# Kernel tuning notes

Measured on AMD Instinct MI355X. Metric: run time of the kernel, lower is better.

Reference implementation:

```python
import jax, jax.numpy as jnp
import numpy as np

T, B, I, H, L = 1024, 64, 512, 512, 2


def _gru_layer(x_seq, h0, w_ih, w_hh, b_ih, b_hh):
    # x_seq: [T, B, in], h0: [B, H]
    # Precompute input-side gates for all timesteps in one big GEMM.
    gx = jnp.einsum('tbi,gi->tbg', x_seq, w_ih) + b_ih  # [T, B, 3H]

    def step(h, gx_t):
        gh = h @ w_hh.T + b_hh                 # [B, 3H]
        i_r, i_z, i_n = jnp.split(gx_t, 3, axis=-1)
        h_r, h_z, h_n = jnp.split(gh, 3, axis=-1)
        r = jax.nn.sigmoid(i_r + h_r)
        z = jax.nn.sigmoid(i_z + h_z)
        n = jnp.tanh(i_n + r * h_n)
        hy = n + z * (h - n)                   # newgate + inputgate*(hx - newgate)
        return hy, hy

    hT, out = jax.lax.scan(step, h0, gx)
    return out, hT  # out: [T, B, H]


def setup_inputs() -> dict:
    key = jax.random.key(0)
    ks = jax.random.split(key, 10)
    stdv = 1.0 / np.sqrt(H)
    u = lambda k, shp: jax.random.uniform(k, shp, jnp.float32, -stdv, stdv)
    return {
        'x': jax.random.normal(ks[0], (T, B, I), jnp.float32),
        'hx': jax.random.normal(ks[1], (L, B, H), jnp.float32),
        'w_ih_0': u(ks[2], (3 * H, I)),
        'w_hh_0': u(ks[3], (3 * H, H)),
        'b_ih_0': u(ks[4], (3 * H,)),
        'b_hh_0': u(ks[5], (3 * H,)),
        'w_ih_1': u(ks[6], (3 * H, H)),
        'w_hh_1': u(ks[7], (3 * H, H)),
        'b_ih_1': u(ks[8], (3 * H,)),
        'b_hh_1': u(ks[9], (3 * H,)),
    }


def reference(x, hx, w_ih_0, w_hh_0, b_ih_0, b_hh_0, w_ih_1, w_hh_1, b_ih_1, b_hh_1):
    out0, h0T = _gru_layer(x, hx[0], w_ih_0, w_hh_0, b_ih_0, b_hh_0)
    out1, h1T = _gru_layer(out0, hx[1], w_ih_1, w_hh_1, b_ih_1, b_hh_1)
    output = out1                         # [T, B, H] (batch_first=False)
    output_hs = jnp.stack([h0T, h1T], 0)  # [L, B, H]
    return output, output_hs
```

## Files before the change

kernel.cpp:

```cpp
#include <hip/hip_runtime.h>
#include <cstdint>
#include <cstddef>

#define T_N 1024
#define B_N 64
#define I_N 512
#define H_N 512
#define G3  (3*H_N)
#define NBLK 256

typedef _Float16 f16;
typedef _Float16 f16x2 __attribute__((ext_vector_type(2)));
typedef unsigned long long ull;

#define SLOT(d) (((d)+2)&1)
#define TAG1(d) ((((d)+2)>>1)&1)

__device__ __forceinline__ f16x2 mkh2(float a, float b) {
  f16x2 v; v.x = (_Float16)a; v.y = (_Float16)b; return v;
}
__device__ __forceinline__ f16x2 bch2(unsigned int u) {
  return __builtin_bit_cast(f16x2, u);
}
__device__ __forceinline__ float fdot2_(f16x2 a, f16x2 b, float c) {
#if __has_builtin(__builtin_amdgcn_fdot2)
  return __builtin_amdgcn_fdot2(a, b, c, false);
#else
  return fmaf((float)a.x, (float)b.x, fmaf((float)a.y, (float)b.y, c));
#endif
}
__device__ __forceinline__ float sigm_(float x) { return 1.f / (1.f + __expf(-x)); }
__device__ __forceinline__ float tanhf_(float x) {
  float xx = fminf(15.f, fmaxf(-15.f, x));
  float e = __expf(2.f * xx);
  return (e - 1.f) / (e + 1.f);
}

__global__ __launch_bounds__(256) void gemm_nt(
    const float* __restrict__ A,
    const float* __restrict__ W,
    const float* __restrict__ bias,
    float* __restrict__ C,
    int M, int N, int K)
{
  __shared__ float As[32][68];
  __shared__ float Ws[32][68];
  const int tid = threadIdx.x;
  const int n0 = blockIdx.x * 64;
  const int m0 = blockIdx.y * 64;
  const int ty = tid >> 4;
  const int tx = tid & 15;

  float acc[4][4];
#pragma unroll
  for (int i = 0; i < 4; ++i)
#pragma unroll
    for (int jj = 0; jj < 4; ++jj) acc[i][jj] = 0.f;

  for (int k0 = 0; k0 < K; k0 += 32) {
#pragma unroll
    for (int i = 0; i < 2; ++i) {
      int idx = tid + i * 256;
      int r   = idx >> 3;
      int c4  = idx & 7;
      float4 va = *(const float4*)(A + (size_t)(m0 + r) * K + k0 + c4 * 4);
      As[c4*4+0][r] = va.x; As[c4*4+1][r] = va.y;
      As[c4*4+2][r] = va.z; As[c4*4+3][r] = va.w;
      float4 vw = *(const float4*)(W + (size_t)(n0 + r) * K + k0 + c4 * 4);
      Ws[c4*4+0][r] = vw.x; Ws[c4*4+1][r] = vw.y;
      Ws[c4*4+2][r] = vw.z; Ws[c4*4+3][r] = vw.w;
    }
    __syncthreads();
#pragma unroll
    for (int k = 0; k < 32; ++k) {
      float4 a = *(const float4*)&As[k][ty * 4];
      float4 w = *(const float4*)&Ws[k][tx * 4];
      acc[0][0] += a.x*w.x; acc[0][1] += a.x*w.y; acc[0][2] += a.x*w.z; acc[0][3] += a.x*w.w;
      acc[1][0] += a.y*w.x; acc[1][1] += a.y*w.y; acc[1][2] += a.y*w.z; acc[1][3] += a.y*w.w;
      acc[2][0] += a.z*w.x; acc[2][1] += a.z*w.y; acc[2][2] += a.z*w.z; acc[2][3] += a.z*w.w;
      acc[3][0] += a.w*w.x; acc[3][1] += a.w*w.y; acc[3][2] += a.w*w.z; acc[3][3] += a.w*w.w;
    }
    __syncthreads();
  }

  float4 bv = *(const float4*)(bias + n0 + tx * 4);
#pragma unroll
  for (int i = 0; i < 4; ++i) {
    int row = m0 + ty * 4 + i;
    float4 o;
    o.x = acc[i][0] + bv.x; o.y = acc[i][1] + bv.y;
    o.z = acc[i][2] + bv.z; o.w = acc[i][3] + bv.w;
    *(float4*)(C + (size_t)row * N + n0 + tx * 4) = o;
  }
}

__global__ __launch_bounds__(256) void pack_h_init(
    const float* __restrict__ hx, f16* __restrict__ h0x, f16* __restrict__ h1x)
{
  int i = blockIdx.x * 256 + threadIdx.x;
  unsigned short a = __builtin_bit_cast(unsigned short, (f16)hx[i]) & 0xFFFEu;
  unsigned short b = __builtin_bit_cast(unsigned short, (f16)hx[B_N * H_N + i]) & 0xFFFEu;
  ((unsigned short*)h0x)[B_N * H_N + i] = a;
  ((unsigned short*)h1x)[B_N * H_N + i] = b;
}

__global__ __launch_bounds__(256) void conv_w(
    const float* __restrict__ whh0, const float* __restrict__ wih1,
    const float* __restrict__ whh1, uint4* __restrict__ wbuf)
{
  int gid = blockIdx.x * 256 + threadIdx.x;
  int idx = gid % 36, rem = gid / 36;
  int tid = rem % 256, j = rem / 256;
  int u = tid >> 4, s = tid & 15;
  int mat = idx / 12, q = (idx % 12) / 4, c = idx % 4;
  const float* src = mat == 0 ? whh0 : (mat == 1 ? wih1 : whh1);
  const float* p = src + (size_t)(q * H_N + 16 * j + u) * H_N + 8 * s + 128 * c;
  uint4 o;
  o.x = __builtin_bit_cast(unsigned int, mkh2(p[0], p[1]));
  o.y = __builtin_bit_cast(unsigned int, mkh2(p[2], p[3]));
  o.z = __builtin_bit_cast(unsigned int, mkh2(p[4], p[5]));
  o.w = __builtin_bit_cast(unsigned int, mkh2(p[6], p[7]));
  wbuf[gid] = o;
}

#define D4Q(acc, wv, vv)                               \
  acc = fdot2_(bch2((wv).x), bch2((vv).x), acc);       \
  acc = fdot2_(bch2((wv).y), bch2((vv).y), acc);       \
  acc = fdot2_(bch2((wv).z), bch2((vv).z), acc);       \
  acc = fdot2_(bch2((wv).w), bch2((vv).w), acc);

template <int NQ>
__device__ __forceinline__ void rscat8(float a[][8], float* r, int s) {
#pragma unroll
  for (int q = 0; q < NQ; ++q) {
    float k4[4];
#pragma unroll
    for (int i = 0; i < 4; ++i) {
      float snd = (s & 1) ? a[q][i] : a[q][4 + i];
      float kp  = (s & 1) ? a[q][4 + i] : a[q][i];
      k4[i] = kp + __shfl_xor(snd, 1);
    }
    float k2[2];
#pragma unroll
    for (int i = 0; i < 2; ++i) {
      float snd = (s & 2) ? k4[i] : k4[2 + i];
      float kp  = (s & 2) ? k4[2 + i] : k4[i];
      k2[i] = kp + __shfl_xor(snd, 2);
    }
    float snd = (s & 4) ? k2[0] : k2[1];
    float kp  = (s & 4) ? k2[1] : k2[0];
    float k1 = kp + __shfl_xor(snd, 4);
    r[q] = k1 + __shfl_xor(k1, 8);
  }
}

__global__ __launch_bounds__(256, 1) void gru_fused(
    const float* __restrict__ gx,
    const float* __restrict__ hx,
    const uint4* __restrict__ wbuf,
    const float* __restrict__ bih1, const float* __restrict__ bhh0,
    const float* __restrict__ bhh1,
    float* __restrict__ out,
    float* __restrict__ hT,
    f16* __restrict__ h0x, f16* __restrict__ h1x)
{
  __shared__ __align__(16) ull sh0q[2][1024];
  __shared__ __align__(16) ull sh1q[1024];
  __shared__ __align__(8) unsigned short pkA[128], pkB[128];

  const int tid = threadIdx.x;
  const int bid = blockIdx.x;
  const int g = bid & 7;
  const int j = bid >> 3;
  const int u = tid >> 4;
  const int s = tid & 15;
  const ull M = 0x0001000100010001ULL;

  uint4 wq[36];
  {
    const uint4* wp = wbuf + ((size_t)j * 256 + tid) * 36;
#pragma unroll
    for (int i = 0; i < 36; ++i) wq[i] = wp[i];
#pragma unroll
    for (int i = 0; i < 36; ++i)
      asm volatile("" : "+v"(wq[i].x), "+v"(wq[i].y), "+v"(wq[i].z), "+v"(wq[i].w));
  }

  const int bb   = 4 * (s & 1) + 2 * ((s >> 1) & 1) + ((s >> 2) & 1);
  const int unit = 16 * j + u;
  const int gbi  = 8 * g + bb;
  const float bR0 = bhh0[unit], bZ0 = bhh0[H_N + unit], bN0 = bhh0[2 * H_N + unit];
  const float bR1 = bih1[unit] + bhh1[unit];
  const float bZ1 = bih1[H_N + unit] + bhh1[H_N + unit];
  const float bN1x = bih1[2 * H_N + unit], bN1h = bhh1[2 * H_N + unit];
  float hv0 = hx[(size_t)gbi * H_N + unit];
  float hv1 = hx[(size_t)(B_N + gbi) * H_N + unit];

  for (int t = 0; t <= T_N + 1; ++t) {
    const bool runA = (t < T_N);
    const bool pollH0 = (t <= T_N);
    const bool runB = (t >= 2);
    const int cur = t & 1;

    const ull* s0 = (const ull*)h0x + (size_t)SLOT(t - 1) * 8192 + (size_t)(8 * g) * 128;
    const ull* s1 = (const ull*)h1x + (size_t)SLOT(t - 3) * 8192 + (size_t)(8 * g) * 128;
    const ull e0 = TAG1(t - 1) ? M : 0ULL;
    const ull e1 = TAG1(t - 3) ? M : 0ULL;
    ull v0[4], v1[4];
    bool k0[4] = {false, false, false, false};
    if (pollH0) {
#pragma unroll
      for (int e = 0; e < 4; ++e)
        v0[e] = __hip_atomic_load(s0 + e * 256 + tid, __ATOMIC_RELAXED, __HIP_MEMORY_SCOPE_AGENT);
    }
    if (runB) {
#pragma unroll
      for (int e = 0; e < 4; ++e)
        v1[e] = __hip_atomic_load(s1 + e * 256 + tid, __ATOMIC_RELAXED, __HIP_MEMORY_SCOPE_AGENT);
    }

    float ir0 = 0, iz0 = 0, in0 = 0;
    if (runA) {
      const float* p = gx + ((size_t)t * B_N + gbi) * G3 + unit;
      ir0 = p[0]; iz0 = p[H_N]; in0 = p[2 * H_N];
    }

    if (runB) {
      bool k1[4] = {false, false, false, false};
      for (;;) {
        bool all = true;
#pragma unroll
        for (int e = 0; e < 4; ++e) {
          if (!k1[e]) k1[e] = ((v1[e] & M) == e1);
          all = all && k1[e];
        }
        if (__all(all)) break;
        __builtin_amdgcn_s_sleep(1);
#pragma unroll
        for (int e = 0; e < 4; ++e)
          if (!k1[e]) v1[e] = __hip_atomic_load(s1 + e * 256 + tid, __ATOMIC_RELAXED, __HIP_MEMORY_SCOPE_AGENT);
      }
#pragma unroll
      for (int e = 0; e < 4; ++e) sh1q[e * 256 + tid] = v1[e];
    }
    __syncthreads();

    if (runB) {
      float aB[4][8];
#pragma unroll
      for (int q = 0; q < 4; ++q)
#pragma unroll
        for (int b8 = 0; b8 < 8; ++b8) aB[q][b8] = 0.f;
      const uint4* xp = (const uint4*)sh0q[cur ^ 1];
      const uint4* hp = (const uint4*)sh1q;
#pragma unroll
      for (int b8 = 0; b8 < 8; ++b8) {
        uint4 xc[4], hc[4];
#pragma unroll
        for (int c = 0; c < 4; ++c) { xc[c] = xp[b8 * 64 + s + 16 * c]; hc[c] = hp[b8 * 64 + s + 16 * c]; }
        float a0 = aB[0][b8], a1 = aB[1][b8], a2 = aB[2][b8], a3 = aB[3][b8];
#pragma unroll
        for (int c = 0; c < 4; ++c) {
          D4Q(a0, wq[12 + 0 * 4 + c], xc[c]); D4Q(a0, wq[24 + 0 * 4 + c], hc[c]);
          D4Q(a1, wq[12 + 1 * 4 + c], xc[c]); D4Q(a1, wq[24 + 1 * 4 + c], hc[c]);
          D4Q(a2, wq[12 + 2 * 4 + c], xc[c]);
          D4Q(a3, wq[24 + 2 * 4 + c], hc[c]);
        }
        aB[0][b8] = a0; aB[1][b8] = a1; aB[2][b8] = a2; aB[3][b8] = a3;
      }
      float rB[4];
      rscat8<4>(aB, rB, s);
      float r = sigm_(rB[0] + bR1);
      float z = sigm_(rB[1] + bZ1);
      float n = tanhf_(rB[2] + bN1x + r * (rB[3] + bN1h));
      float hy = n + z * (hv1 - n); hv1 = hy;
      if (s < 8) pkB[bb * 16 + u] = __builtin_bit_cast(unsigned short, (f16)hy);
    }

    if (pollH0) {
      for (;;) {
        bool all = true;
#pragma unroll
        for (int e = 0; e < 4; ++e) {
          if (!k0[e]) k0[e] = ((v0[e] & M) == e0);
          all = all && k0[e];
        }
        if (__all(all)) break;
        __builtin_amdgcn_s_sleep(1);
#pragma unroll
        for (int e = 0; e < 4; ++e)
          if (!k0[e]) v0[e] = __hip_atomic_load(s0 + e * 256 + tid, __ATOMIC_RELAXED, __HIP_MEMORY_SCOPE_AGENT);
      }
#pragma unroll
      for (int e = 0; e < 4; ++e) sh0q[cur][e * 256 + tid] = v0[e];
    }
    __syncthreads();

    if (runA) {
      float aA[3][8];
#pragma unroll
      for (int q = 0; q < 3; ++q)
#pragma unroll
        for (int b8 = 0; b8 < 8; ++b8) aA[q][b8] = 0.f;
      const uint4* xp = (const uint4*)sh0q[cur];
#pragma unroll
      for (int b8 = 0; b8 < 8; ++b8) {
        uint4 xc[4];
#pragma unroll
        for (int c = 0; c < 4; ++c) xc[c] = xp[b8 * 64 + s + 16 * c];
        float a0 = aA[0][b8], a1 = aA[1][b8], a2 = aA[2][b8];
#pragma unroll
        for (int c = 0; c < 4; ++c) {
          D4Q(a0, wq[0 * 4 + c], xc[c]);
          D4Q(a1, wq[1 * 4 + c], xc[c]);
          D4Q(a2, wq[2 * 4 + c], xc[c]);
        }
        aA[0][b8] = a0; aA[1][b8] = a1; aA[2][b8] = a2;
      }
      float rA[3];
      rscat8<3>(aA, rA, s);
      float r = sigm_(ir0 + rA[0] + bR0);
      float z = sigm_(iz0 + rA[1] + bZ0);
      float n = tanhf_(in0 + r * (rA[2] + bN0));
      float hy = n + z * (hv0 - n); hv0 = hy;
      if (s < 8) {
        pkA[bb * 16 + u] = __builtin_bit_cast(unsigned short, (f16)hy);
        if (t == T_N - 1) hT[(size_t)gbi * H_N + unit] = hy;
      }
    }
    __syncthreads();

    if (tid < 32) {
      if (runA) {
        ull v = ((const ull*)pkA)[tid];
        v = (v & ~M) | (TAG1(t) ? M : 0ULL);
        ull* dp = (ull*)h0x + (size_t)SLOT(t) * 8192
                + (size_t)(8 * g + (tid >> 2)) * 128 + 4 * j + (tid & 3);
        __hip_atomic_store(dp, v, __ATOMIC_RELAXED, __HIP_MEMORY_SCOPE_AGENT);
      }
    } else if (tid < 64) {
      if (runB) {
        const int l = tid - 32;
        ull v = ((const ull*)pkB)[l];
        f16x2 p0 = bch2((unsigned int)v), p1 = bch2((unsigned int)(v >> 32));
        float4 o = {(float)p0.x, (float)p0.y, (float)p1.x, (float)p1.y};
        float* op = out + ((size_t)(t - 2) * B_N + 8 * g + (l >> 2)) * H_N + 16 * j + 4 * (l & 3);
        *(float4*)op = o;
        if (t == T_N + 1)
          *(float4*)(hT + (size_t)(B_N + 8 * g + (l >> 2)) * H_N + 16 * j + 4 * (l & 3)) = o;
        if (t <= T_N) {
          v = (v & ~M) | (TAG1(t - 2) ? M : 0ULL);
          ull* dp = (ull*)h1x + (size_t)SLOT(t - 2) * 8192
                  + (size_t)(8 * g + (l >> 2)) * 128 + 4 * j + (l & 3);
          __hip_atomic_store(dp, v, __ATOMIC_RELAXED, __HIP_MEMORY_SCOPE_AGENT);
        }
      }
    }
  }
}

extern "C" void kernel_launch(void* const* d_in, const int* in_sizes, int n_in,
                              void* d_out, int out_size, void* d_ws, size_t ws_size,
                              hipStream_t stream)
{
  const float* x    = (const float*)d_in[0];
  const float* hx   = (const float*)d_in[1];
  const float* wih0 = (const float*)d_in[2];
  const float* whh0 = (const float*)d_in[3];
  const float* bih0 = (const float*)d_in[4];
  const float* bhh0 = (const float*)d_in[5];
  const float* wih1 = (const float*)d_in[6];
  const float* whh1 = (const float*)d_in[7];
  const float* bih1 = (const float*)d_in[8];
  const float* bhh1 = (const float*)d_in[9];
  float* out = (float*)d_out;

  float* gxb = (float*)d_ws;
  f16*   h0x = (f16*)(gxb + (size_t)T_N * B_N * G3);
  f16*   h1x = h0x + 2 * B_N * H_N;
  uint4* wbuf = (uint4*)(h1x + 2 * B_N * H_N);

  pack_h_init<<<128, 256, 0, stream>>>(hx, h0x, h1x);
  conv_w<<<(32 * 256 * 36) / 256, 256, 0, stream>>>(whh0, wih1, whh1, wbuf);

  dim3 gg(G3 / 64, (T_N * B_N) / 64);
  gemm_nt<<<gg, 256, 0, stream>>>(x, wih0, bih0, gxb, T_N * B_N, G3, I_N);

  gru_fused<<<NBLK, 256, 0, stream>>>(gxb, hx, wbuf,
                                      bih1, bhh0, bhh1,
                                      out, out + (size_t)T_N * B_N * H_N,
                                      h0x, h1x);
}
```

Before: 8.917 ms.

## Split GRU recurrence reduction across 512 threads with half the weights per thread

Each block of the persistent fused GRU kernel now runs 512 threads instead of 256. The per-thread register-resident weight slice shrinks from 36 to 18 uint4, and each hidden unit's dot product is split across 32 lanes instead of 16. The weight-packing kernel, the shared-memory access pattern and the shuffle reduction change to match, and the reduction gains one more xor-16 stage. The aim is to shorten the serial per-timestep dot-product chain and free registers for more latency hiding, at the cost of an extra shuffle level, more threads synchronising at each barrier, and more lanes sitting idle during the activation step.

```diff
diff --git a/kernel.cpp b/kernel.cpp
--- a/kernel.cpp
+++ b/kernel.cpp
@@ -109,12 +109,12 @@
     const float* __restrict__ whh1, uint4* __restrict__ wbuf)
 {
   int gid = blockIdx.x * 256 + threadIdx.x;
-  int idx = gid % 36, rem = gid / 36;
-  int tid = rem % 256, j = rem / 256;
-  int u = tid >> 4, s = tid & 15;
-  int mat = idx / 12, q = (idx % 12) / 4, c = idx % 4;
+  int idx = gid % 18, rem = gid / 18;
+  int tid = rem % 512, j = rem / 512;
+  int u = tid >> 5, s = tid & 31;
+  int mat = idx / 6, q = (idx % 6) / 2, c = idx % 2;
   const float* src = mat == 0 ? whh0 : (mat == 1 ? wih1 : whh1);
-  const float* p = src + (size_t)(q * H_N + 16 * j + u) * H_N + 8 * s + 128 * c;
+  const float* p = src + (size_t)(q * H_N + 16 * j + u) * H_N + 16 * s + 8 * c;
   uint4 o;
   o.x = __builtin_bit_cast(unsigned int, mkh2(p[0], p[1]));
   o.y = __builtin_bit_cast(unsigned int, mkh2(p[2], p[3]));
@@ -130,7 +130,7 @@
   acc = fdot2_(bch2((wv).w), bch2((vv).w), acc);
 
 template <int NQ>
-__device__ __forceinline__ void rscat8(float a[][8], float* r, int s) {
+__device__ __forceinline__ void rscat8w(float a[][8], float* r, int s) {
 #pragma unroll
   for (int q = 0; q < NQ; ++q) {
     float k4[4];
@@ -150,11 +150,12 @@
     float snd = (s & 4) ? k2[0] : k2[1];
     float kp  = (s & 4) ? k2[1] : k2[0];
     float k1 = kp + __shfl_xor(snd, 4);
-    r[q] = k1 + __shfl_xor(k1, 8);
-  }
-}
-
-__global__ __launch_bounds__(256, 1) void gru_fused(
+    k1 = k1 + __shfl_xor(k1, 8);
+    r[q] = k1 + __shfl_xor(k1, 16);
+  }
+}
+
+__global__ __launch_bounds__(512, 2) void gru_fused(
     const float* __restrict__ gx,
     const float* __restrict__ hx,
     const uint4* __restrict__ wbuf,
@@ -172,29 +173,34 @@
   const int bid = blockIdx.x;
   const int g = bid & 7;
   const int j = bid >> 3;
-  const int u = tid >> 4;
-  const int s = tid & 15;
+  const int u = tid >> 5;
+  const int s = tid & 31;
   const ull M = 0x0001000100010001ULL;
 
-  uint4 wq[36];
+  uint4 wq[18];
   {
-    const uint4* wp = wbuf + ((size_t)j * 256 + tid) * 36;
-#pragma unroll
-    for (int i = 0; i < 36; ++i) wq[i] = wp[i];
-#pragma unroll
-    for (int i = 0; i < 36; ++i)
+    const uint4* wp = wbuf + ((size_t)j * 512 + tid) * 18;
+#pragma unroll
+    for (int i = 0; i < 18; ++i) wq[i] = wp[i];
+#pragma unroll
+    for (int i = 0; i < 18; ++i)
       asm volatile("" : "+v"(wq[i].x), "+v"(wq[i].y), "+v"(wq[i].z), "+v"(wq[i].w));
   }
 
   const int bb   = 4 * (s & 1) + 2 * ((s >> 1) & 1) + ((s >> 2) & 1);
   const int unit = 16 * j + u;
   const int gbi  = 8 * g + bb;
-  const float bR0 = bhh0[unit], bZ0 = bhh0[H_N + unit], bN0 = bhh0[2 * H_N + unit];
-  const float bR1 = bih1[unit] + bhh1[unit];
-  const float bZ1 = bih1[H_N + unit] + bhh1[H_N + unit];
-  const float bN1x = bih1[2 * H_N + unit], bN1h = bhh1[2 * H_N + unit];
-  float hv0 = hx[(size_t)gbi * H_N + unit];
-  float hv1 = hx[(size_t)(B_N + gbi) * H_N + unit];
+  const bool wr  = (s < 8);
+  float bR0 = 0, bZ0 = 0, bN0 = 0, bR1 = 0, bZ1 = 0, bN1x = 0, bN1h = 0;
+  float hv0 = 0, hv1 = 0;
+  if (wr) {
+    bR0 = bhh0[unit]; bZ0 = bhh0[H_N + unit]; bN0 = bhh0[2 * H_N + unit];
+    bR1 = bih1[unit] + bhh1[unit];
+    bZ1 = bih1[H_N + unit] + bhh1[H_N + unit];
+    bN1x = bih1[2 * H_N + unit]; bN1h = bhh1[2 * H_N + unit];
+    hv0 = hx[(size_t)gbi * H_N + unit];
+    hv1 = hx[(size_t)(B_N + gbi) * H_N + unit];
+  }
 
   for (int t = 0; t <= T_N + 1; ++t) {
     const bool runA = (t < T_N);
@@ -206,42 +212,42 @@
     const ull* s1 = (const ull*)h1x + (size_t)SLOT(t - 3) * 8192 + (size_t)(8 * g) * 128;
     const ull e0 = TAG1(t - 1) ? M : 0ULL;
     const ull e1 = TAG1(t - 3) ? M : 0ULL;
-    ull v0[4], v1[4];
-    bool k0[4] = {false, false, false, false};
+    ull v0[2], v1[2];
+    bool k0[2] = {false, false};
     if (pollH0) {
 #pragma unroll
-      for (int e = 0; e < 4; ++e)
-        v0[e] = __hip_atomic_load(s0 + e * 256 + tid, __ATOMIC_RELAXED, __HIP_MEMORY_SCOPE_AGENT);
+      for (int e = 0; e < 2; ++e)
+        v0[e] = __hip_atomic_load(s0 + e * 512 + tid, __ATOMIC_RELAXED, __HIP_MEMORY_SCOPE_AGENT);
     }
     if (runB) {
 #pragma unroll
-      for (int e = 0; e < 4; ++e)
-        v1[e] = __hip_atomic_load(s1 + e * 256 + tid, __ATOMIC_RELAXED, __HIP_MEMORY_SCOPE_AGENT);
+      for (int e = 0; e < 2; ++e)
+        v1[e] = __hip_atomic_load(s1 + e * 512 + tid, __ATOMIC_RELAXED, __HIP_MEMORY_SCOPE_AGENT);
     }
 
     float ir0 = 0, iz0 = 0, in0 = 0;
-    if (runA) {
+    if (runA && wr) {
       const float* p = gx + ((size_t)t * B_N + gbi) * G3 + unit;
       ir0 = p[0]; iz0 = p[H_N]; in0 = p[2 * H_N];
     }
 
     if (runB) {
-      bool k1[4] = {false, false, false, false};
+      bool k1[2] = {false, false};
       for (;;) {
         bool all = true;
 #pragma unroll
-        for (int e = 0; e < 4; ++e) {
+        for (int e = 0; e < 2; ++e) {
           if (!k1[e]) k1[e] = ((v1[e] & M) == e1);
           all = all && k1[e];
         }
         if (__all(all)) break;
         __builtin_amdgcn_s_sleep(1);
 #pragma unroll
-        for (int e = 0; e < 4; ++e)
-          if (!k1[e]) v1[e] = __hip_atomic_load(s1 + e * 256 + tid, __ATOMIC_RELAXED, __HIP_MEMORY_SCOPE_AGENT);
-      }
-#pragma unroll
-      for (int e = 0; e < 4; ++e) sh1q[e * 256 + tid] = v1[e];
+        for (int e = 0; e < 2; ++e)
+          if (!k1[e]) v1[e] = __hip_atomic_load(s1 + e * 512 + tid, __ATOMIC_RELAXED, __HIP_MEMORY_SCOPE_AGENT);
+      }
+#pragma unroll
+      for (int e = 0; e < 2; ++e) sh1q[e * 512 + tid] = v1[e];
     }
     __syncthreads();
 
@@ -255,44 +261,49 @@
       const uint4* hp = (const uint4*)sh1q;
 #pragma unroll
       for (int b8 = 0; b8 < 8; ++b8) {
-        uint4 xc[4], hc[4];
-#pragma unroll
-        for (int c = 0; c < 4; ++c) { xc[c] = xp[b8 * 64 + s + 16 * c]; hc[c] = hp[b8 * 64 + s + 16 * c]; }
+        uint4 xc[2], hc[2];
+#pragma unroll
+        for (int c = 0; c < 2; ++c) {
+          xc[c] = xp[b8 * 64 + 2 * s + c];
+          hc[c] = hp[b8 * 64 + 2 * s + c];
+        }
         float a0 = aB[0][b8], a1 = aB[1][b8], a2 = aB[2][b8], a3 = aB[3][b8];
 #pragma unroll
-        for (int c = 0; c < 4; ++c) {
-          D4Q(a0, wq[12 + 0 * 4 + c], xc[c]); D4Q(a0, wq[24 + 0 * 4 + c], hc[c]);
-          D4Q(a1, wq[12 + 1 * 4 + c], xc[c]); D4Q(a1, wq[24 + 1 * 4 + c], hc[c]);
-          D4Q(a2, wq[12 + 2 * 4 + c], xc[c]);
-          D4Q(a3, wq[24 + 2 * 4 + c], hc[c]);
+        for (int c = 0; c < 2; ++c) {
+          D4Q(a0, wq[6 + c],  xc[c]); D4Q(a0, wq[12 + c], hc[c]);
+          D4Q(a1, wq[8 + c],  xc[c]); D4Q(a1, wq[14 + c], hc[c]);
+          D4Q(a2, wq[10 + c], xc[c]);
+          D4Q(a3, wq[16 + c], hc[c]);
         }
         aB[0][b8] = a0; aB[1][b8] = a1; aB[2][b8] = a2; aB[3][b8] = a3;
       }
       float rB[4];
-      rscat8<4>(aB, rB, s);
-      float r = sigm_(rB[0] + bR1);
-      float z = sigm_(rB[1] + bZ1);
-      float n = tanhf_(rB[2] + bN1x + r * (rB[3] + bN1h));
-      float hy = n + z * (hv1 - n); hv1 = hy;
-      if (s < 8) pkB[bb * 16 + u] = __builtin_bit_cast(unsigned short, (f16)hy);
+      rscat8w<4>(aB, rB, s);
+      if (wr) {
+        float r = sigm_(rB[0] + bR1);
+        float z = sigm_(rB[1] + bZ1);
+        float n = tanhf_(rB[2] + bN1x + r * (rB[3] + bN1h));
+        float hy = n + z * (hv1 - n); hv1 = hy;
+        pkB[bb * 16 + u] = __builtin_bit_cast(unsigned short, (f16)hy);
+      }
     }
 
     if (pollH0) {
       for (;;) {
         bool all = true;
 #pragma unroll
-        for (int e = 0; e < 4; ++e) {
+        for (int e = 0; e < 2; ++e) {
           if (!k0[e]) k0[e] = ((v0[e] & M) == e0);
           all = all && k0[e];
         }
         if (__all(all)) break;
         __builtin_amdgcn_s_sleep(1);
 #pragma unroll
-        for (int e = 0; e < 4; ++e)
-          if (!k0[e]) v0[e] = __hip_atomic_load(s0 + e * 256 + tid, __ATOMIC_RELAXED, __HIP_MEMORY_SCOPE_AGENT);
-      }
-#pragma unroll
-      for (int e = 0; e < 4; ++e) sh0q[cur][e * 256 + tid] = v0[e];
+        for (int e = 0; e < 2; ++e)
+          if (!k0[e]) v0[e] = __hip_atomic_load(s0 + e * 512 + tid, __ATOMIC_RELAXED, __HIP_MEMORY_SCOPE_AGENT);
+      }
+#pragma unroll
+      for (int e = 0; e < 2; ++e) sh0q[cur][e * 512 + tid] = v0[e];
     }
     __syncthreads();
 
@@ -305,25 +316,25 @@
       const uint4* xp = (const uint4*)sh0q[cur];
 #pragma unroll
       for (int b8 = 0; b8 < 8; ++b8) {
-        uint4 xc[4];
-#pragma unroll
-        for (int c = 0; c < 4; ++c) xc[c] = xp[b8 * 64 + s + 16 * c];
+        uint4 xc[2];
+        xc[0] = xp[b8 * 64 + 2 * s];
+        xc[1] = xp[b8 * 64 + 2 * s + 1];
         float a0 = aA[0][b8], a1 = aA[1][b8], a2 = aA[2][b8];
 #pragma unroll
-        for (int c = 0; c < 4; ++c) {
-          D4Q(a0, wq[0 * 4 + c], xc[c]);
-          D4Q(a1, wq[1 * 4 + c], xc[c]);
-          D4Q(a2, wq[2 * 4 + c], xc[c]);
+        for (int c = 0; c < 2; ++c) {
+          D4Q(a0, wq[0 + c], xc[c]);
+          D4Q(a1, wq[2 + c], xc[c]);
+          D4Q(a2, wq[4 + c], xc[c]);
         }
         aA[0][b8] = a0; aA[1][b8] = a1; aA[2][b8] = a2;
       }
       float rA[3];
-      rscat8<3>(aA, rA, s);
-      float r = sigm_(ir0 + rA[0] + bR0);
-      float z = sigm_(iz0 + rA[1] + bZ0);
-      float n = tanhf_(in0 + r * (rA[2] + bN0));
-      float hy = n + z * (hv0 - n); hv0 = hy;
-      if (s < 8) {
+      rscat8w<3>(aA, rA, s);
+      if (wr) {
+        float r = sigm_(ir0 + rA[0] + bR0);
+        float z = sigm_(iz0 + rA[1] + bZ0);
+        float n = tanhf_(in0 + r * (rA[2] + bN0));
+        float hy = n + z * (hv0 - n); hv0 = hy;
         pkA[bb * 16 + u] = __builtin_bit_cast(unsigned short, (f16)hy);
         if (t == T_N - 1) hT[(size_t)gbi * H_N + unit] = hy;
       }
@@ -381,12 +392,12 @@
   uint4* wbuf = (uint4*)(h1x + 2 * B_N * H_N);
 
   pack_h_init<<<128, 256, 0, stream>>>(hx, h0x, h1x);
-  conv_w<<<(32 * 256 * 36) / 256, 256, 0, stream>>>(whh0, wih1, whh1, wbuf);
+  conv_w<<<(32 * 512 * 18) / 256, 256, 0, stream>>>(whh0, wih1, whh1, wbuf);
 
   dim3 gg(G3 / 64, (T_N * B_N) / 64);
   gemm_nt<<<gg, 256, 0, stream>>>(x, wih0, bih0, gxb, T_N * B_N, G3, I_N);
 
-  gru_fused<<<NBLK, 256, 0, stream>>>(gxb, hx, wbuf,
+  gru_fused<<<NBLK, 512, 0, stream>>>(gxb, hx, wbuf,
                                       bih1, bhh0, bhh1,
                                       out, out + (size_t)T_N * B_N * H_N,
                                       h0x, h1x);
```

After: 10.01 ms. 12.2% more time.

## Split fused two-layer GRU into separate layer-0 and layer-1 block groups

Applied to the files above, without the earlier changes.

The persistent kernel now launches 512 blocks: half run layer 0 and half run layer 1, each holding only its own weights in registers, instead of every block interleaving both layers per step. The hidden-state exchange buffers grow from 2 to 8 slots, so layer 0 can run up to several steps ahead of layer 1, with a throttle poll on layer-1 progress to stop slot reuse. This aims to shorten each block's per-step critical path and lower register pressure, which allows more occupancy. The cost is twice as many resident blocks spinning on global flags, and the design relies on all 512 blocks being co-resident to avoid deadlock.

```diff
diff --git a/kernel.cpp b/kernel.cpp
--- a/kernel.cpp
+++ b/kernel.cpp
@@ -7,14 +7,13 @@
 #define I_N 512
 #define H_N 512
 #define G3  (3*H_N)
-#define NBLK 256
 
 typedef _Float16 f16;
 typedef _Float16 f16x2 __attribute__((ext_vector_type(2)));
 typedef unsigned long long ull;
 
-#define SLOT(d) (((d)+2)&1)
-#define TAG1(d) ((((d)+2)>>1)&1)
+#define S8(d) (((d)+8)&7)
+#define T8(d) ((((d)+8)>>3)&1)
 
 __device__ __forceinline__ f16x2 mkh2(float a, float b) {
   f16x2 v; v.x = (_Float16)a; v.y = (_Float16)b; return v;
@@ -100,8 +99,8 @@
   int i = blockIdx.x * 256 + threadIdx.x;
   unsigned short a = __builtin_bit_cast(unsigned short, (f16)hx[i]) & 0xFFFEu;
   unsigned short b = __builtin_bit_cast(unsigned short, (f16)hx[B_N * H_N + i]) & 0xFFFEu;
-  ((unsigned short*)h0x)[B_N * H_N + i] = a;
-  ((unsigned short*)h1x)[B_N * H_N + i] = b;
+  ((unsigned short*)h0x)[7 * B_N * H_N + i] = a;
+  ((unsigned short*)h1x)[7 * B_N * H_N + i] = b;
 }
 
 __global__ __launch_bounds__(256) void conv_w(
@@ -154,7 +153,23 @@
   }
 }
 
-__global__ __launch_bounds__(256, 1) void gru_fused(
+#define POLL4(vv, kk, sp, ee)                                                  \
+  for (;;) {                                                                   \
+    bool all_ = true;                                                          \
+    _Pragma("unroll")                                                          \
+    for (int e_ = 0; e_ < 4; ++e_) {                                           \
+      if (!kk[e_]) kk[e_] = ((vv[e_] & M) == ee);                              \
+      all_ = all_ && kk[e_];                                                   \
+    }                                                                          \
+    if (__all(all_)) break;                                                    \
+    __builtin_amdgcn_s_sleep(1);                                               \
+    _Pragma("unroll")                                                          \
+    for (int e_ = 0; e_ < 4; ++e_)                                             \
+      if (!kk[e_]) vv[e_] = __hip_atomic_load(sp + e_ * 256 + tid,             \
+                     __ATOMIC_RELAXED, __HIP_MEMORY_SCOPE_AGENT);              \
+  }
+
+__global__ __launch_bounds__(256) void gru_split(
     const float* __restrict__ gx,
     const float* __restrict__ hx,
     const uint4* __restrict__ wbuf,
@@ -164,196 +179,200 @@
     float* __restrict__ hT,
     f16* __restrict__ h0x, f16* __restrict__ h1x)
 {
-  __shared__ __align__(16) ull sh0q[2][1024];
+  __shared__ __align__(16) ull shq[1024];
   __shared__ __align__(16) ull sh1q[1024];
-  __shared__ __align__(8) unsigned short pkA[128], pkB[128];
+  __shared__ __align__(8) unsigned short pk[128];
 
   const int tid = threadIdx.x;
-  const int bid = blockIdx.x;
-  const int g = bid & 7;
-  const int j = bid >> 3;
+  const bool L0 = (blockIdx.x < 256);
+  const int lb = L0 ? blockIdx.x : blockIdx.x - 256;
+  const int g = lb & 7;
+  const int j = lb >> 3;
   const int u = tid >> 4;
   const int s = tid & 15;
   const ull M = 0x0001000100010001ULL;
 
-  uint4 wq[36];
-  {
-    const uint4* wp = wbuf + ((size_t)j * 256 + tid) * 36;
-#pragma unroll
-    for (int i = 0; i < 36; ++i) wq[i] = wp[i];
-#pragma unroll
-    for (int i = 0; i < 36; ++i)
-      asm volatile("" : "+v"(wq[i].x), "+v"(wq[i].y), "+v"(wq[i].z), "+v"(wq[i].w));
-  }
-
   const int bb   = 4 * (s & 1) + 2 * ((s >> 1) & 1) + ((s >> 2) & 1);
   const int unit = 16 * j + u;
   const int gbi  = 8 * g + bb;
-  const float bR0 = bhh0[unit], bZ0 = bhh0[H_N + unit], bN0 = bhh0[2 * H_N + unit];
-  const float bR1 = bih1[unit] + bhh1[unit];
-  const float bZ1 = bih1[H_N + unit] + bhh1[H_N + unit];
-  const float bN1x = bih1[2 * H_N + unit], bN1h = bhh1[2 * H_N + unit];
-  float hv0 = hx[(size_t)gbi * H_N + unit];
-  float hv1 = hx[(size_t)(B_N + gbi) * H_N + unit];
-
-  for (int t = 0; t <= T_N + 1; ++t) {
-    const bool runA = (t < T_N);
-    const bool pollH0 = (t <= T_N);
-    const bool runB = (t >= 2);
-    const int cur = t & 1;
-
-    const ull* s0 = (const ull*)h0x + (size_t)SLOT(t - 1) * 8192 + (size_t)(8 * g) * 128;
-    const ull* s1 = (const ull*)h1x + (size_t)SLOT(t - 3) * 8192 + (size_t)(8 * g) * 128;
-    const ull e0 = TAG1(t - 1) ? M : 0ULL;
-    const ull e1 = TAG1(t - 3) ? M : 0ULL;
-    ull v0[4], v1[4];
-    bool k0[4] = {false, false, false, false};
-    if (pollH0) {
+  const bool wr  = (s < 8);
+  const ull* h0u = (const ull*)h0x;
+  const ull* h1u = (const ull*)h1x;
+
+  if (L0) {
+    uint4 wq[12];
+    {
+      const uint4* wp = wbuf + ((size_t)j * 256 + tid) * 36;
+#pragma unroll
+      for (int i = 0; i < 12; ++i) wq[i] = wp[i];
+#pragma unroll
+      for (int i = 0; i < 12; ++i)
+        asm volatile("" : "+v"(wq[i].x), "+v"(wq[i].y), "+v"(wq[i].z), "+v"(wq[i].w));
+    }
+    float bR0 = 0, bZ0 = 0, bN0 = 0, hv0 = 0;
+    if (wr) {
+      bR0 = bhh0[unit]; bZ0 = bhh0[H_N + unit]; bN0 = bhh0[2 * H_N + unit];
+      hv0 = hx[(size_t)gbi * H_N + unit];
+    }
+
+    for (int t = 0; t < T_N; ++t) {
+      const ull* s0 = h0u + (size_t)S8(t - 1) * 8192 + (size_t)(8 * g) * 128;
+      const ull e0 = T8(t - 1) ? M : 0ULL;
+      ull v0[4]; bool k0[4] = {false, false, false, false};
 #pragma unroll
       for (int e = 0; e < 4; ++e)
         v0[e] = __hip_atomic_load(s0 + e * 256 + tid, __ATOMIC_RELAXED, __HIP_MEMORY_SCOPE_AGENT);
-    }
-    if (runB) {
-#pragma unroll
-      for (int e = 0; e < 4; ++e)
+      const bool thr = (t >= 7);
+      const ull* sT = h1u + (size_t)S8(t - 7) * 8192 + (size_t)(8 * g) * 128;
+      const ull eT = T8(t - 7) ? M : 0ULL;
+      ull vT[4]; bool kT[4] = {!thr, !thr, !thr, !thr};
+      if (thr) {
+#pragma unroll
+        for (int e = 0; e < 4; ++e)
+          vT[e] = __hip_atomic_load(sT + e * 256 + tid, __ATOMIC_RELAXED, __HIP_MEMORY_SCOPE_AGENT);
+      }
+      float ir0 = 0, iz0 = 0, in0 = 0;
+      if (wr) {
+        const float* p = gx + ((size_t)t * B_N + gbi) * G3 + unit;
+        ir0 = p[0]; iz0 = p[H_N]; in0 = p[2 * H_N];
+      }
+
+      POLL4(v0, k0, s0, e0)
+#pragma unroll
+      for (int e = 0; e < 4; ++e) shq[e * 256 + tid] = v0[e];
+      __syncthreads();
+
+      float aA[3][8];
+#pragma unroll
+      for (int q = 0; q < 3; ++q)
+#pragma unroll
+        for (int b8 = 0; b8 < 8; ++b8) aA[q][b8] = 0.f;
+      const uint4* xp = (const uint4*)shq;
+#pragma unroll
+      for (int b8 = 0; b8 < 8; ++b8) {
+        uint4 xc[4];
+#pragma unroll
+        for (int c = 0; c < 4; ++c) xc[c] = xp[b8 * 64 + s + 16 * c];
+        float a0 = aA[0][b8], a1 = aA[1][b8], a2 = aA[2][b8];
+#pragma unroll
+        for (int c = 0; c < 4; ++c) {
+          D4Q(a0, wq[0 + c], xc[c]);
+          D4Q(a1, wq[4 + c], xc[c]);
+          D4Q(a2, wq[8 + c], xc[c]);
+        }
+        aA[0][b8] = a0; aA[1][b8] = a1; aA[2][b8] = a2;
+      }
+      float rA[3];
+      rscat8<3>(aA, rA, s);
+      if (wr) {
+        float r = sigm_(ir0 + rA[0] + bR0);
+        float z = sigm_(iz0 + rA[1] + bZ0);
+        float n = tanhf_(in0 + r * (rA[2] + bN0));
+        float hy = n + z * (hv0 - n); hv0 = hy;
+        pk[bb * 16 + u] = __builtin_bit_cast(unsigned short, (f16)hy);
+        if (t == T_N - 1) hT[(size_t)gbi * H_N + unit] = hy;
+      }
+      POLL4(vT, kT, sT, eT)
+      __syncthreads();
+
+      if (tid < 32) {
+        ull v = ((const ull*)pk)[tid];
+        v = (v & ~M) | (T8(t) ? M : 0ULL);
+        ull* dp = (ull*)h0x + (size_t)S8(t) * 8192
+                + (size_t)(8 * g + (tid >> 2)) * 128 + 4 * j + (tid & 3);
+        __hip_atomic_store(dp, v, __ATOMIC_RELAXED, __HIP_MEMORY_SCOPE_AGENT);
+      }
+    }
+  } else {
+    uint4 wq[24];
+    {
+      const uint4* wp = wbuf + ((size_t)j * 256 + tid) * 36;
+#pragma unroll
+      for (int i = 0; i < 24; ++i) wq[i] = wp[12 + i];
+#pragma unroll
+      for (int i = 0; i < 24; ++i)
+        asm volatile("" : "+v"(wq[i].x), "+v"(wq[i].y), "+v"(wq[i].z), "+v"(wq[i].w));
+    }
+    float bR1 = 0, bZ1 = 0, bN1x = 0, bN1h = 0, hv1 = 0;
+    if (wr) {
+      bR1 = bih1[unit] + bhh1[unit];
+      bZ1 = bih1[H_N + unit] + bhh1[H_N + unit];
+      bN1x = bih1[2 * H_N + unit]; bN1h = bhh1[2 * H_N + unit];
+      hv1 = hx[(size_t)(B_N + gbi) * H_N + unit];
+    }
+
+    for (int t = 0; t < T_N; ++t) {
+      const ull* s1 = h1u + (size_t)S8(t - 1) * 8192 + (size_t)(8 * g) * 128;
+      const ull e1 = T8(t - 1) ? M : 0ULL;
+      const ull* s0 = h0u + (size_t)S8(t) * 8192 + (size_t)(8 * g) * 128;
+      const ull e0 = T8(t) ? M : 0ULL;
+      ull v1[4], v0[4];
+      bool k1[4] = {false, false, false, false};
+      bool k0[4] = {false, false, false, false};
+#pragma unroll
+      for (int e = 0; e < 4; ++e) {
         v1[e] = __hip_atomic_load(s1 + e * 256 + tid, __ATOMIC_RELAXED, __HIP_MEMORY_SCOPE_AGENT);
-    }
-
-    float ir0 = 0, iz0 = 0, in0 = 0;
-    if (runA) {
-      const float* p = gx + ((size_t)t * B_N + gbi) * G3 + unit;
-      ir0 = p[0]; iz0 = p[H_N]; in0 = p[2 * H_N];
-    }
-
-    if (runB) {
-      bool k1[4] = {false, false, false, false};
-      for (;;) {
-        bool all = true;
-#pragma unroll
-        for (int e = 0; e < 4; ++e) {
-          if (!k1[e]) k1[e] = ((v1[e] & M) == e1);
-          all = all && k1[e];
-        }
-        if (__all(all)) break;
-        __builtin_amdgcn_s_sleep(1);
-#pragma unroll
-        for (int e = 0; e < 4; ++e)
-          if (!k1[e]) v1[e] = __hip_atomic_load(s1 + e * 256 + tid, __ATOMIC_RELAXED, __HIP_MEMORY_SCOPE_AGENT);
-      }
+        v0[e] = __hip_atomic_load(s0 + e * 256 + tid, __ATOMIC_RELAXED, __HIP_MEMORY_SCOPE_AGENT);
+      }
+      POLL4(v1, k1, s1, e1)
 #pragma unroll
       for (int e = 0; e < 4; ++e) sh1q[e * 256 + tid] = v1[e];
-    }
-    __syncthreads();
-
-    if (runB) {
+      POLL4(v0, k0, s0, e0)
+#pragma unroll
+      for (int e = 0; e < 4; ++e) shq[e * 256 + tid] = v0[e];
+      __syncthreads();
+
       float aB[4][8];
 #pragma unroll
       for (int q = 0; q < 4; ++q)
 #pragma unroll
         for (int b8 = 0; b8 < 8; ++b8) aB[q][b8] = 0.f;
-      const uint4* xp = (const uint4*)sh0q[cur ^ 1];
+      const uint4* xp = (const uint4*)shq;
       const uint4* hp = (const uint4*)sh1q;
 #pragma unroll
       for (int b8 = 0; b8 < 8; ++b8) {
         uint4 xc[4], hc[4];
 #pragma unroll
-        for (int c = 0; c < 4; ++c) { xc[c] = xp[b8 * 64 + s + 16 * c]; hc[c] = hp[b8 * 64 + s + 16 * c]; }
+        for (int c = 0; c < 4; ++c) {
+          xc[c] = xp[b8 * 64 + s + 16 * c];
+          hc[c] = hp[b8 * 64 + s + 16 * c];
+        }
         float a0 = aB[0][b8], a1 = aB[1][b8], a2 = aB[2][b8], a3 = aB[3][b8];
 #pragma unroll
         for (int c = 0; c < 4; ++c) {
-          D4Q(a0, wq[12 + 0 * 4 + c], xc[c]); D4Q(a0, wq[24 + 0 * 4 + c], hc[c]);
-          D4Q(a1, wq[12 + 1 * 4 + c], xc[c]); D4Q(a1, wq[24 + 1 * 4 + c], hc[c]);
-          D4Q(a2, wq[12 + 2 * 4 + c], xc[c]);
-          D4Q(a3, wq[24 + 2 * 4 + c], hc[c]);
+          D4Q(a0, wq[0 + c], xc[c]);  D4Q(a0, wq[12 + c], hc[c]);
+          D4Q(a1, wq[4 + c], xc[c]);  D4Q(a1, wq[16 + c], hc[c]);
+          D4Q(a2, wq[8 + c], xc[c]);
+          D4Q(a3, wq[20 + c], hc[c]);
         }
         aB[0][b8] = a0; aB[1][b8] = a1; aB[2][b8] = a2; aB[3][b8] = a3;
       }
       float rB[4];
       rscat8<4>(aB, rB, s);
-      float r = sigm_(rB[0] + bR1);
-      float z = sigm_(rB[1] + bZ1);
-      float n = tanhf_(rB[2] + bN1x + r * (rB[3] + bN1h));
-      float hy = n + z * (hv1 - n); hv1 = hy;
-      if (s < 8) pkB[bb * 16 + u] = __builtin_bit_cast(unsigned short, (f16)hy);
-    }
-
-    if (pollH0) {
-      for (;;) {
-        bool all = true;
-#pragma unroll
-        for (int e = 0; e < 4; ++e) {
-          if (!k0[e]) k0[e] = ((v0[e] & M) == e0);
-          all = all && k0[e];
-        }
-        if (__all(all)) break;
-        __builtin_amdgcn_s_sleep(1);
-#pragma unroll
-        for (int e = 0; e < 4; ++e)
-          if (!k0[e]) v0[e] = __hip_atomic_load(s0 + e * 256 + tid, __ATOMIC_RELAXED, __HIP_MEMORY_SCOPE_AGENT);
-      }
-#pragma unroll
-      for (int e = 0; e < 4; ++e) sh0q[cur][e * 256 + tid] = v0[e];
-    }
-    __syncthreads();
-
-    if (runA) {
-      float aA[3][8];
-#pragma unroll
-      for (int q = 0; q < 3; ++q)
-#pragma unroll
-        for (int b8 = 0; b8 < 8; ++b8) aA[q][b8] = 0.f;
-      const uint4* xp = (const uint4*)sh0q[cur];
-#pragma unroll
-      for (int b8 = 0; b8 < 8; ++b8) {
-        uint4 xc[4];
-#pragma unroll
-        for (int c = 0; c < 4; ++c) xc[c] = xp[b8 * 64 + s + 16 * c];
-        float a0 = aA[0][b8], a1 = aA[1][b8], a2 = aA[2][b8];
-#pragma unroll
-        for (int c = 0; c < 4; ++c) {
-          D4Q(a0, wq[0 * 4 + c], xc[c]);
-          D4Q(a1, wq[1 * 4 + c], xc[c]);
-          D4Q(a2, wq[2 * 4 + c], xc[c]);
-        }
-        aA[0][b8] = a0; aA[1][b8] = a1; aA[2][b8] = a2;
-      }
-      float rA[3];
-      rscat8<3>(aA, rA, s);
-      float r = sigm_(ir0 + rA[0] + bR0);
-      float z = sigm_(iz0 + rA[1] + bZ0);
-      float n = tanhf_(in0 + r * (rA[2] + bN0));
-      float hy = n + z * (hv0 - n); hv0 = hy;
-      if (s < 8) {
-        pkA[bb * 16 + u] = __builtin_bit_cast(unsigned short, (f16)hy);
-        if (t == T_N - 1) hT[(size_t)gbi * H_N + unit] = hy;
-      }
-    }
-    __syncthreads();
-
-    if (tid < 32) {
-      if (runA) {
-        ull v = ((const ull*)pkA)[tid];
-        v = (v & ~M) | (TAG1(t) ? M : 0ULL);
-        ull* dp = (ull*)h0x + (size_t)SLOT(t) * 8192
+      if (wr) {
+        float r = sigm_(rB[0] + bR1);
+        float z = sigm_(rB[1] + bZ1);
+        float n = tanhf_(rB[2] + bN1x + r * (rB[3] + bN1h));
+        float hy = n + z * (hv1 - n); hv1 = hy;
+        pk[bb * 16 + u] = __builtin_bit_cast(unsigned short, (f16)hy);
+      }
+      __syncthreads();
+
+      if (tid < 32) {
+        ull v = ((const ull*)pk)[tid];
+        v = (v & ~M) | (T8(t) ? M : 0ULL);
+        ull* dp = (ull*)h1x + (size_t)S8(t) * 8192
                 + (size_t)(8 * g + (tid >> 2)) * 128 + 4 * j + (tid & 3);
         __hip_atomic_store(dp, v, __ATOMIC_RELAXED, __HIP_MEMORY_SCOPE_AGENT);
-      }
-    } else if (tid < 64) {
-      if (runB) {
+      } else if (tid < 64) {
         const int l = tid - 32;
-        ull v = ((const ull*)pkB)[l];
+        ull v = ((const ull*)pk)[l];
         f16x2 p0 = bch2((unsigned int)v), p1 = bch2((unsigned int)(v >> 32));
         float4 o = {(float)p0.x, (float)p0.y, (float)p1.x, (float)p1.y};
-        float* op = out + ((size_t)(t - 2) * B_N + 8 * g + (l >> 2)) * H_N + 16 * j + 4 * (l & 3);
+        float* op = out + ((size_t)t * B_N + 8 * g + (l >> 2)) * H_N + 16 * j + 4 * (l & 3);
         *(float4*)op = o;
-        if (t == T_N + 1)
+        if (t == T_N - 1)
           *(float4*)(hT + (size_t)(B_N + 8 * g + (l >> 2)) * H_N + 16 * j + 4 * (l & 3)) = o;
-        if (t <= T_N) {
-          v = (v & ~M) | (TAG1(t - 2) ? M : 0ULL);
-          ull* dp = (ull*)h1x + (size_t)SLOT(t - 2) * 8192
-                  + (size_t)(8 * g + (l >> 2)) * 128 + 4 * j + (l & 3);
-          __hip_atomic_store(dp, v, __ATOMIC_RELAXED, __HIP_MEMORY_SCOPE_AGENT);
-        }
       }
     }
   }
@@ -377,8 +396,8 @@
 
   float* gxb = (float*)d_ws;
   f16*   h0x = (f16*)(gxb + (size_t)T_N * B_N * G3);
-  f16*   h1x = h0x + 2 * B_N * H_N;
-  uint4* wbuf = (uint4*)(h1x + 2 * B_N * H_N);
+  f16*   h1x = h0x + 8 * B_N * H_N;
+  uint4* wbuf = (uint4*)(h1x + 8 * B_N * H_N);
 
   pack_h_init<<<128, 256, 0, stream>>>(hx, h0x, h1x);
   conv_w<<<(32 * 256 * 36) / 256, 256, 0, stream>>>(whh0, wih1, whh1, wbuf);
@@ -386,8 +405,8 @@
   dim3 gg(G3 / 64, (T_N * B_N) / 64);
   gemm_nt<<<gg, 256, 0, stream>>>(x, wih0, bih0, gxb, T_N * B_N, G3, I_N);
 
-  gru_fused<<<NBLK, 256, 0, stream>>>(gxb, hx, wbuf,
-                                      bih1, bhh0, bhh1,
-                                      out, out + (size_t)T_N * B_N * H_N,
-                                      h0x, h1x);
-}
+  gru_split<<<512, 256, 0, stream>>>(gxb, hx, wbuf,
+                                     bih1, bhh0, bhh1,
+                                     out, out + (size_t)T_N * B_N * H_N,
+                                     h0x, h1x);
+}
```

New measurement: 10.75 ms. 20.6% more time.
